# Optimization experiments

Measured on AMD Instinct MI355X. Metric: run time of the kernel, lower is better.

## Reference

```python
import jax, jax.numpy as jnp
import numpy as np

B, L, H, C = 2, 512, 128, 25

def setup_inputs() -> dict:
    key = jax.random.key(0)
    k1, k2, k3, k4 = jax.random.split(key, 4)
    x1 = jax.random.normal(k1, (B, L, H), dtype=jnp.float32)
    x2 = jax.random.normal(k2, (B, L, H), dtype=jnp.float32)
    W = jax.random.normal(k3, (C, 4 * H), dtype=jnp.float32) * (1.0 / np.sqrt(4 * H))
    b = jax.random.normal(k4, (C,), dtype=jnp.float32) * 0.01
    return {"x1": x1, "x2": x2, "W": W, "b": b}

def reference(x1, x2, W, b):
    # feat = cat([x1_i, x2_j, x1_i*x2_j, |x1_i - x2_j|]) over all (i, j) pairs,
    # then Linear(4H -> C). Split W into its 4 H-sized blocks so we never
    # materialize the [B, L, L, 4H] concatenated tensor.
    Hd = x1.shape[-1]
    W1, W2, W3, W4 = (W[:, 0:Hd], W[:, Hd:2*Hd], W[:, 2*Hd:3*Hd], W[:, 3*Hd:4*Hd])
    a = x1[:, :, None, :]   # [B, L, 1, H] -> row token
    c = x2[:, None, :, :]   # [B, 1, L, H] -> col token
    # a@W1 and c@W2 depend on only one index, so compute [B, L, C] then broadcast.
    t1 = jnp.einsum('blh,ch->blc', x1, W1)[:, :, None, :]  # [B, L, 1, C]
    t2 = jnp.einsum('blh,ch->blc', x2, W2)[:, None, :, :]  # [B, 1, L, C]
    # product term is a bilinear contraction; no [B,L,L,H] materialization needed.
    t3 = jnp.einsum('blh,bmh,ch->blmc', x1, x2, W3)         # [B, L, L, C]
    # abs-diff term requires the pairwise [B, L, L, H] tensor (nonlinear in pair).
    t4 = jnp.einsum('blmh,ch->blmc', jnp.abs(a - c), W4)    # [B, L, L, C]
    return t1 + t2 + t3 + t4 + b  # [B, L, L, C]
```

## Files before the change

### kernel.cpp

```cpp
#include <hip/hip_runtime.h>
#include <hip/hip_bf16.h>
#include <math.h>

#define BB 2
#define LL 512
#define HH 128
#define CC 25
#define W4H (4*HH)

typedef __attribute__((ext_vector_type(4))) float    f32x4;
typedef __attribute__((ext_vector_type(8))) _Float16 half8;
typedef __attribute__((ext_vector_type(2))) _Float16 half2t;
typedef __attribute__((ext_vector_type(4))) unsigned uint4v;

#define MTILE 64
#define LPB   8
#define XPH   136

static __device__ __forceinline__ half8 habs8(half8 x) {
    uint4v u = __builtin_bit_cast(uint4v, x);
    u &= 0x7FFF7FFFu;
    return __builtin_bit_cast(half8, u);
}
static __device__ __forceinline__ half2t pkrtz(float a, float b) {
    return __builtin_bit_cast(half2t, __builtin_amdgcn_cvt_pkrtz(a, b));
}
union H4 { half2t h2[2]; unsigned long long u64; };
union H8 { half2t h2[4]; uint4v u4; half8 h8; };

__global__ __launch_bounds__(256)
void biaffine_fused(const float* __restrict__ x1, const float* __restrict__ x2,
                    const float* __restrict__ W, const float* __restrict__ bias,
                    float* __restrict__ out)
{
    __shared__ __align__(16) _Float16 wfrag[2048 * 8];
    __shared__ __align__(16) _Float16 x2h[MTILE * XPH];
    __shared__ __align__(16) _Float16 x1h[LPB * XPH];

    const int tid = threadIdx.x;
    const int b   = blockIdx.z;
    const int l0  = blockIdx.y * LPB;
    const int m0  = blockIdx.x * MTILE;

    const int lane = tid & 63;
    const int wv   = tid >> 6;
    const int q    = lane >> 4;
    const int cn   = lane & 15;

    #pragma unroll
    for (int i = 0; i < 8; ++i) {
        const int fid = i * 256 + tid;
        const int ln  = fid & 63;
        const int t   = (fid >> 6) & 1;
        const int kk  = fid >> 7;
        const int c   = (ln & 15) + 16 * t;
        const int k0  = kk * 32 + ((ln >> 4) << 3);
        const int wc  = (k0 + 256) & 511;
        H8 h; h.u4 = (uint4v){0u, 0u, 0u, 0u};
        if (c < CC) {
            const f32x4 v0 = *(const f32x4*)(W + (size_t)c * W4H + wc);
            const f32x4 v1 = *(const f32x4*)(W + (size_t)c * W4H + wc + 4);
            h.h2[0] = pkrtz(v0[0], v0[1]);
            h.h2[1] = pkrtz(v0[2], v0[3]);
            h.h2[2] = pkrtz(v1[0], v1[1]);
            h.h2[3] = pkrtz(v1[2], v1[3]);
        }
        *(uint4v*)(&wfrag[fid * 8]) = h.u4;
    }

    {
        const float* sx2 = x2 + ((size_t)b * LL + m0) * HH;
        #pragma unroll
        for (int i = 0; i < 8; ++i) {
            const int idx = i * 256 + tid;
            const int r   = idx >> 5;
            const int c4  = idx & 31;
            const f32x4 v = *(const f32x4*)(sx2 + r * HH + c4 * 4);
            H4 h;
            h.h2[0] = pkrtz(v[0], v[1]);
            h.h2[1] = pkrtz(v[2], v[3]);
            *(unsigned long long*)(&x2h[r * XPH + c4 * 4]) = h.u64;
        }
        const float* sx1 = x1 + ((size_t)b * LL + l0) * HH;
        const int r  = tid >> 5;
        const int c4 = tid & 31;
        const f32x4 v = *(const f32x4*)(sx1 + r * HH + c4 * 4);
        H4 h;
        h.h2[0] = pkrtz(v[0], v[1]);
        h.h2[1] = pkrtz(v[2], v[3]);
        *(unsigned long long*)(&x1h[r * XPH + c4 * 4]) = h.u64;
    }
    __syncthreads();

    half8 Bf0[16], Bf1[16];
    #pragma unroll
    for (int kk = 0; kk < 16; ++kk) {
        Bf0[kk] = *(const half8*)(&wfrag[((kk * 2 + 0) * 64 + lane) * 8]);
        Bf1[kk] = *(const half8*)(&wfrag[((kk * 2 + 1) * 64 + lane) * 8]);
    }

    const int mrowA = wv * 16 + cn;
    half8 X2f[4];
    #pragma unroll
    for (int hh = 0; hh < 4; ++hh)
        X2f[hh] = *(const half8*)(&x2h[mrowA * XPH + hh * 32 + q * 8]);

    const float ba = bias[cn];
    const float bb = (cn + 16 < CC) ? bias[cn + 16] : 0.f;

    #pragma unroll
    for (int l = 0; l < LPB; ++l) {
        f32x4 acc0 = {0.f, 0.f, 0.f, 0.f};
        f32x4 acc1 = {0.f, 0.f, 0.f, 0.f};

        #pragma unroll
        for (int hh = 0; hh < 4; ++hh) {
            const half8 a  = *(const half8*)(&x1h[l * XPH + hh * 32 + q * 8]);
            const half8 bq = X2f[hh];
            const half8 Ap = a * bq;
            const half8 Ad = habs8(a - bq);
            acc0 = __builtin_amdgcn_mfma_f32_16x16x32_f16(Ap, Bf0[hh],      acc0, 0, 0, 0);
            acc1 = __builtin_amdgcn_mfma_f32_16x16x32_f16(Ap, Bf1[hh],      acc1, 0, 0, 0);
            acc0 = __builtin_amdgcn_mfma_f32_16x16x32_f16(Ad, Bf0[4 + hh],  acc0, 0, 0, 0);
            acc1 = __builtin_amdgcn_mfma_f32_16x16x32_f16(Ad, Bf1[4 + hh],  acc1, 0, 0, 0);
            acc0 = __builtin_amdgcn_mfma_f32_16x16x32_f16(a,  Bf0[8 + hh],  acc0, 0, 0, 0);
            acc1 = __builtin_amdgcn_mfma_f32_16x16x32_f16(a,  Bf1[8 + hh],  acc1, 0, 0, 0);
            acc0 = __builtin_amdgcn_mfma_f32_16x16x32_f16(bq, Bf0[12 + hh], acc0, 0, 0, 0);
            acc1 = __builtin_amdgcn_mfma_f32_16x16x32_f16(bq, Bf1[12 + hh], acc1, 0, 0, 0);
        }

        const int lg = l0 + l;
        #pragma unroll
        for (int r = 0; r < 4; ++r) {
            const int mg = m0 + wv * 16 + q * 4 + r;
            float* o = out + (((size_t)b * LL + lg) * LL + mg) * CC;
            o[cn] = acc0[r] + ba;
            if (cn + 16 < CC) o[cn + 16] = acc1[r] + bb;
        }
    }
}

extern "C" void kernel_launch(void* const* d_in, const int* in_sizes, int n_in,
                              void* d_out, int out_size, void* d_ws, size_t ws_size,
                              hipStream_t stream) {
    const float* x1   = (const float*)d_in[0];
    const float* x2   = (const float*)d_in[1];
    const float* W    = (const float*)d_in[2];
    const float* bias = (const float*)d_in[3];
    float* out = (float*)d_out;

    dim3 grid(LL / MTILE, LL / LPB, BB);
    biaffine_fused<<<grid, 256, 0, stream>>>(x1, x2, W, bias, out);
}
```

Before: 92.33 us.

## Prepack W fragments in a separate kernel and split channel halves to cut LDS/registers

Moves the fp16 packing of W into a small pre-kernel that writes MFMA-ready fragments to workspace, so the main kernel no longer spends 32KB of LDS and a per-block conversion on W. The main kernel now loops over the two 16-channel halves sequentially, loading only 16 B-fragments at a time from global memory, which halves register pressure and allows launch_bounds(256,4) for higher occupancy. The trade-off is an extra launch, recomputing the A operands (product and abs-diff) twice, and splitting the output stores into two passes with less contiguity.

```diff
diff --git a/kernel.cpp b/kernel.cpp
--- a/kernel.cpp
+++ b/kernel.cpp
@@ -28,12 +28,34 @@
 union H4 { half2t h2[2]; unsigned long long u64; };
 union H8 { half2t h2[4]; uint4v u4; half8 h8; };
 
+
 __global__ __launch_bounds__(256)
+void wpack_kernel(const float* __restrict__ W, _Float16* __restrict__ wsWf)
+{
+    const int fid = blockIdx.x * 256 + threadIdx.x;
+    const int ln  = fid & 63;
+    const int t   = (fid >> 6) & 1;
+    const int kk  = fid >> 7;
+    const int c   = (ln & 15) + 16 * t;
+    const int k0  = kk * 32 + ((ln >> 4) << 3);
+    const int wc  = (k0 + 256) & 511;
+    H8 h; h.u4 = (uint4v){0u, 0u, 0u, 0u};
+    if (c < CC) {
+        const f32x4 v0 = *(const f32x4*)(W + (size_t)c * W4H + wc);
+        const f32x4 v1 = *(const f32x4*)(W + (size_t)c * W4H + wc + 4);
+        h.h2[0] = pkrtz(v0[0], v0[1]);
+        h.h2[1] = pkrtz(v0[2], v0[3]);
+        h.h2[2] = pkrtz(v1[0], v1[1]);
+        h.h2[3] = pkrtz(v1[2], v1[3]);
+    }
+    *(uint4v*)(wsWf + (size_t)fid * 8) = h.u4;
+}
+
+__global__ __launch_bounds__(256, 4)
 void biaffine_fused(const float* __restrict__ x1, const float* __restrict__ x2,
-                    const float* __restrict__ W, const float* __restrict__ bias,
+                    const _Float16* __restrict__ wsWf, const float* __restrict__ bias,
                     float* __restrict__ out)
 {
-    __shared__ __align__(16) _Float16 wfrag[2048 * 8];
     __shared__ __align__(16) _Float16 x2h[MTILE * XPH];
     __shared__ __align__(16) _Float16 x1h[LPB * XPH];
 
@@ -46,27 +68,6 @@
     const int wv   = tid >> 6;
     const int q    = lane >> 4;
     const int cn   = lane & 15;
-
-    #pragma unroll
-    for (int i = 0; i < 8; ++i) {
-        const int fid = i * 256 + tid;
-        const int ln  = fid & 63;
-        const int t   = (fid >> 6) & 1;
-        const int kk  = fid >> 7;
-        const int c   = (ln & 15) + 16 * t;
-        const int k0  = kk * 32 + ((ln >> 4) << 3);
-        const int wc  = (k0 + 256) & 511;
-        H8 h; h.u4 = (uint4v){0u, 0u, 0u, 0u};
-        if (c < CC) {
-            const f32x4 v0 = *(const f32x4*)(W + (size_t)c * W4H + wc);
-            const f32x4 v1 = *(const f32x4*)(W + (size_t)c * W4H + wc + 4);
-            h.h2[0] = pkrtz(v0[0], v0[1]);
-            h.h2[1] = pkrtz(v0[2], v0[3]);
-            h.h2[2] = pkrtz(v1[0], v1[1]);
-            h.h2[3] = pkrtz(v1[2], v1[3]);
-        }
-        *(uint4v*)(&wfrag[fid * 8]) = h.u4;
-    }
 
     {
         const float* sx2 = x2 + ((size_t)b * LL + m0) * HH;
@@ -92,50 +93,46 @@
     }
     __syncthreads();
 
-    half8 Bf0[16], Bf1[16];
-    #pragma unroll
-    for (int kk = 0; kk < 16; ++kk) {
-        Bf0[kk] = *(const half8*)(&wfrag[((kk * 2 + 0) * 64 + lane) * 8]);
-        Bf1[kk] = *(const half8*)(&wfrag[((kk * 2 + 1) * 64 + lane) * 8]);
-    }
-
     const int mrowA = wv * 16 + cn;
     half8 X2f[4];
     #pragma unroll
     for (int hh = 0; hh < 4; ++hh)
         X2f[hh] = *(const half8*)(&x2h[mrowA * XPH + hh * 32 + q * 8]);
 
-    const float ba = bias[cn];
-    const float bb = (cn + 16 < CC) ? bias[cn + 16] : 0.f;
+    for (int t = 0; t < 2; ++t) {
+        half8 Bf[16];
+        #pragma unroll
+        for (int kk = 0; kk < 16; ++kk)
+            Bf[kk] = *(const half8*)(wsWf + ((size_t)(kk * 2 + t) * 64 + lane) * 8);
 
-    #pragma unroll
-    for (int l = 0; l < LPB; ++l) {
-        f32x4 acc0 = {0.f, 0.f, 0.f, 0.f};
-        f32x4 acc1 = {0.f, 0.f, 0.f, 0.f};
+        const int  cg   = cn + 16 * t;
+        const bool cok  = (cg < CC);
+        const float bt  = cok ? bias[cg] : 0.f;
 
         #pragma unroll
-        for (int hh = 0; hh < 4; ++hh) {
-            const half8 a  = *(const half8*)(&x1h[l * XPH + hh * 32 + q * 8]);
-            const half8 bq = X2f[hh];
-            const half8 Ap = a * bq;
-            const half8 Ad = habs8(a - bq);
-            acc0 = __builtin_amdgcn_mfma_f32_16x16x32_f16(Ap, Bf0[hh],      acc0, 0, 0, 0);
-            acc1 = __builtin_amdgcn_mfma_f32_16x16x32_f16(Ap, Bf1[hh],      acc1, 0, 0, 0);
-            acc0 = __builtin_amdgcn_mfma_f32_16x16x32_f16(Ad, Bf0[4 + hh],  acc0, 0, 0, 0);
-            acc1 = __builtin_amdgcn_mfma_f32_16x16x32_f16(Ad, Bf1[4 + hh],  acc1, 0, 0, 0);
-            acc0 = __builtin_amdgcn_mfma_f32_16x16x32_f16(a,  Bf0[8 + hh],  acc0, 0, 0, 0);
-            acc1 = __builtin_amdgcn_mfma_f32_16x16x32_f16(a,  Bf1[8 + hh],  acc1, 0, 0, 0);
-            acc0 = __builtin_amdgcn_mfma_f32_16x16x32_f16(bq, Bf0[12 + hh], acc0, 0, 0, 0);
-            acc1 = __builtin_amdgcn_mfma_f32_16x16x32_f16(bq, Bf1[12 + hh], acc1, 0, 0, 0);
-        }
+        for (int l = 0; l < LPB; ++l) {
+            f32x4 acc0 = {0.f, 0.f, 0.f, 0.f};
 
-        const int lg = l0 + l;
-        #pragma unroll
-        for (int r = 0; r < 4; ++r) {
-            const int mg = m0 + wv * 16 + q * 4 + r;
-            float* o = out + (((size_t)b * LL + lg) * LL + mg) * CC;
-            o[cn] = acc0[r] + ba;
-            if (cn + 16 < CC) o[cn + 16] = acc1[r] + bb;
+            #pragma unroll
+            for (int hh = 0; hh < 4; ++hh) {
+                const half8 a  = *(const half8*)(&x1h[l * XPH + hh * 32 + q * 8]);
+                const half8 bq = X2f[hh];
+                const half8 Ap = a * bq;
+                const half8 Ad = habs8(a - bq);
+                acc0 = __builtin_amdgcn_mfma_f32_16x16x32_f16(Ap, Bf[hh],      acc0, 0, 0, 0);
+                acc0 = __builtin_amdgcn_mfma_f32_16x16x32_f16(Ad, Bf[4 + hh],  acc0, 0, 0, 0);
+                acc0 = __builtin_amdgcn_mfma_f32_16x16x32_f16(a,  Bf[8 + hh],  acc0, 0, 0, 0);
+                acc0 = __builtin_amdgcn_mfma_f32_16x16x32_f16(bq, Bf[12 + hh], acc0, 0, 0, 0);
+            }
+
+            const int lg = l0 + l;
+            if (cok) {
+                #pragma unroll
+                for (int r = 0; r < 4; ++r) {
+                    const int mg = m0 + wv * 16 + q * 4 + r;
+                    out[(((size_t)b * LL + lg) * LL + mg) * CC + cg] = acc0[r] + bt;
+                }
+            }
         }
     }
 }
@@ -148,7 +145,10 @@
     const float* W    = (const float*)d_in[2];
     const float* bias = (const float*)d_in[3];
     float* out = (float*)d_out;
+    _Float16* wsWf = (_Float16*)d_ws;
+
+    wpack_kernel<<<8, 256, 0, stream>>>(W, wsWf);
 
     dim3 grid(LL / MTILE, LL / LPB, BB);
-    biaffine_fused<<<grid, 256, 0, stream>>>(x1, x2, W, bias, out);
+    biaffine_fused<<<grid, 256, 0, stream>>>(x1, x2, wsWf, bias, out);
 }
```

Result: slower. 312.3 us (+238.2%).

## Hoist rank-one x1·W1 and x2·W2 terms out of the per-pair MFMA loop

Applied to the files above, without the earlier changes.

The x1·W1 term depends only on the row index and the x2·W2 term only on the column index. The kernel now computes each of them once per block with small MFMA passes: t1 is stored in LDS together with the bias, and t2 is kept in registers. The per-(l, m) inner loop then runs only the product and abs-diff contractions, which halves its MFMA count. W fragments and x2 are also loaded straight from global memory into registers instead of being staged through LDS. This adds an extra barrier and redundant global W loads per wave.

```diff
diff --git a/kernel.cpp b/kernel.cpp
--- a/kernel.cpp
+++ b/kernel.cpp
@@ -28,14 +28,28 @@
 union H4 { half2t h2[2]; unsigned long long u64; };
 union H8 { half2t h2[4]; uint4v u4; half8 h8; };
 
+static __device__ __forceinline__ half8 loadWfrag(const float* __restrict__ W,
+                                                  int c, int col0) {
+    H8 h; h.u4 = (uint4v){0u, 0u, 0u, 0u};
+    if (c < CC) {
+        const float* p = W + (size_t)c * W4H + col0;
+        const f32x4 v0 = *(const f32x4*)(p);
+        const f32x4 v1 = *(const f32x4*)(p + 4);
+        h.h2[0] = pkrtz(v0[0], v0[1]);
+        h.h2[1] = pkrtz(v0[2], v0[3]);
+        h.h2[2] = pkrtz(v1[0], v1[1]);
+        h.h2[3] = pkrtz(v1[2], v1[3]);
+    }
+    return h.h8;
+}
+
 __global__ __launch_bounds__(256)
 void biaffine_fused(const float* __restrict__ x1, const float* __restrict__ x2,
                     const float* __restrict__ W, const float* __restrict__ bias,
                     float* __restrict__ out)
 {
-    __shared__ __align__(16) _Float16 wfrag[2048 * 8];
-    __shared__ __align__(16) _Float16 x2h[MTILE * XPH];
     __shared__ __align__(16) _Float16 x1h[LPB * XPH];
+    __shared__ __align__(16) float    t1s[LPB * 32];
 
     const int tid = threadIdx.x;
     const int b   = blockIdx.z;
@@ -47,40 +61,7 @@
     const int q    = lane >> 4;
     const int cn   = lane & 15;
 
-    #pragma unroll
-    for (int i = 0; i < 8; ++i) {
-        const int fid = i * 256 + tid;
-        const int ln  = fid & 63;
-        const int t   = (fid >> 6) & 1;
-        const int kk  = fid >> 7;
-        const int c   = (ln & 15) + 16 * t;
-        const int k0  = kk * 32 + ((ln >> 4) << 3);
-        const int wc  = (k0 + 256) & 511;
-        H8 h; h.u4 = (uint4v){0u, 0u, 0u, 0u};
-        if (c < CC) {
-            const f32x4 v0 = *(const f32x4*)(W + (size_t)c * W4H + wc);
-            const f32x4 v1 = *(const f32x4*)(W + (size_t)c * W4H + wc + 4);
-            h.h2[0] = pkrtz(v0[0], v0[1]);
-            h.h2[1] = pkrtz(v0[2], v0[3]);
-            h.h2[2] = pkrtz(v1[0], v1[1]);
-            h.h2[3] = pkrtz(v1[2], v1[3]);
-        }
-        *(uint4v*)(&wfrag[fid * 8]) = h.u4;
-    }
-
     {
-        const float* sx2 = x2 + ((size_t)b * LL + m0) * HH;
-        #pragma unroll
-        for (int i = 0; i < 8; ++i) {
-            const int idx = i * 256 + tid;
-            const int r   = idx >> 5;
-            const int c4  = idx & 31;
-            const f32x4 v = *(const f32x4*)(sx2 + r * HH + c4 * 4);
-            H4 h;
-            h.h2[0] = pkrtz(v[0], v[1]);
-            h.h2[1] = pkrtz(v[2], v[3]);
-            *(unsigned long long*)(&x2h[r * XPH + c4 * 4]) = h.u64;
-        }
         const float* sx1 = x1 + ((size_t)b * LL + l0) * HH;
         const int r  = tid >> 5;
         const int c4 = tid & 31;
@@ -92,26 +73,72 @@
     }
     __syncthreads();
 
-    half8 Bf0[16], Bf1[16];
-    #pragma unroll
-    for (int kk = 0; kk < 16; ++kk) {
-        Bf0[kk] = *(const half8*)(&wfrag[((kk * 2 + 0) * 64 + lane) * 8]);
-        Bf1[kk] = *(const half8*)(&wfrag[((kk * 2 + 1) * 64 + lane) * 8]);
+    const int mrowA = wv * 16 + cn;
+    half8 X2f[4];
+    {
+        const float* px2 = x2 + ((size_t)b * LL + m0 + mrowA) * HH;
+        #pragma unroll
+        for (int hh = 0; hh < 4; ++hh) {
+            const float* p = px2 + hh * 32 + q * 8;
+            const f32x4 v0 = *(const f32x4*)(p);
+            const f32x4 v1 = *(const f32x4*)(p + 4);
+            H8 h;
+            h.h2[0] = pkrtz(v0[0], v0[1]);
+            h.h2[1] = pkrtz(v0[2], v0[3]);
+            h.h2[2] = pkrtz(v1[0], v1[1]);
+            h.h2[3] = pkrtz(v1[2], v1[3]);
+            X2f[hh] = h.h8;
+        }
     }
 
-    const int mrowA = wv * 16 + cn;
-    half8 X2f[4];
+    f32x4 t2a = {0.f,0.f,0.f,0.f}, t2b = {0.f,0.f,0.f,0.f};
     #pragma unroll
-    for (int hh = 0; hh < 4; ++hh)
-        X2f[hh] = *(const half8*)(&x2h[mrowA * XPH + hh * 32 + q * 8]);
+    for (int kk = 0; kk < 4; ++kk) {
+        const int col0 = HH + kk * 32 + q * 8;
+        const half8 b0 = loadWfrag(W, cn,      col0);
+        const half8 b1 = loadWfrag(W, cn + 16, col0);
+        t2a = __builtin_amdgcn_mfma_f32_16x16x32_f16(X2f[kk], b0, t2a, 0, 0, 0);
+        t2b = __builtin_amdgcn_mfma_f32_16x16x32_f16(X2f[kk], b1, t2b, 0, 0, 0);
+    }
 
-    const float ba = bias[cn];
-    const float bb = (cn + 16 < CC) ? bias[cn + 16] : 0.f;
+    if (wv == 0) {
+        f32x4 t1acc0 = {0.f,0.f,0.f,0.f}, t1acc1 = {0.f,0.f,0.f,0.f};
+        #pragma unroll
+        for (int kk = 0; kk < 4; ++kk) {
+            const half8 a1 = *(const half8*)(&x1h[(cn & 7) * XPH + kk * 32 + q * 8]);
+            const int col0 = kk * 32 + q * 8;
+            const half8 b0 = loadWfrag(W, cn,      col0);
+            const half8 b1 = loadWfrag(W, cn + 16, col0);
+            t1acc0 = __builtin_amdgcn_mfma_f32_16x16x32_f16(a1, b0, t1acc0, 0, 0, 0);
+            t1acc1 = __builtin_amdgcn_mfma_f32_16x16x32_f16(a1, b1, t1acc1, 0, 0, 0);
+        }
+        if (q < 2) {
+            const float ba = bias[cn];
+            const float bb = (cn + 16 < CC) ? bias[cn + 16] : 0.f;
+            #pragma unroll
+            for (int r = 0; r < 4; ++r) {
+                const int l = q * 4 + r;
+                t1s[l * 32 + cn]      = t1acc0[r] + ba;
+                t1s[l * 32 + 16 + cn] = t1acc1[r] + bb;
+            }
+        }
+    }
+
+    half8 Bf0[8], Bf1[8];
+    #pragma unroll
+    for (int kk = 0; kk < 8; ++kk) {
+        const int col0 = 2 * HH + kk * 32 + q * 8;
+        Bf0[kk] = loadWfrag(W, cn,      col0);
+        Bf1[kk] = loadWfrag(W, cn + 16, col0);
+    }
+    __syncthreads();
+
+    const bool cok = (cn + 16 < CC);
 
     #pragma unroll
     for (int l = 0; l < LPB; ++l) {
-        f32x4 acc0 = {0.f, 0.f, 0.f, 0.f};
-        f32x4 acc1 = {0.f, 0.f, 0.f, 0.f};
+        f32x4 acc0 = {0.f,0.f,0.f,0.f};
+        f32x4 acc1 = {0.f,0.f,0.f,0.f};
 
         #pragma unroll
         for (int hh = 0; hh < 4; ++hh) {
@@ -119,23 +146,20 @@
             const half8 bq = X2f[hh];
             const half8 Ap = a * bq;
             const half8 Ad = habs8(a - bq);
-            acc0 = __builtin_amdgcn_mfma_f32_16x16x32_f16(Ap, Bf0[hh],      acc0, 0, 0, 0);
-            acc1 = __builtin_amdgcn_mfma_f32_16x16x32_f16(Ap, Bf1[hh],      acc1, 0, 0, 0);
-            acc0 = __builtin_amdgcn_mfma_f32_16x16x32_f16(Ad, Bf0[4 + hh],  acc0, 0, 0, 0);
-            acc1 = __builtin_amdgcn_mfma_f32_16x16x32_f16(Ad, Bf1[4 + hh],  acc1, 0, 0, 0);
-            acc0 = __builtin_amdgcn_mfma_f32_16x16x32_f16(a,  Bf0[8 + hh],  acc0, 0, 0, 0);
-            acc1 = __builtin_amdgcn_mfma_f32_16x16x32_f16(a,  Bf1[8 + hh],  acc1, 0, 0, 0);
-            acc0 = __builtin_amdgcn_mfma_f32_16x16x32_f16(bq, Bf0[12 + hh], acc0, 0, 0, 0);
-            acc1 = __builtin_amdgcn_mfma_f32_16x16x32_f16(bq, Bf1[12 + hh], acc1, 0, 0, 0);
+            acc0 = __builtin_amdgcn_mfma_f32_16x16x32_f16(Ap, Bf0[hh],     acc0, 0, 0, 0);
+            acc1 = __builtin_amdgcn_mfma_f32_16x16x32_f16(Ap, Bf1[hh],     acc1, 0, 0, 0);
+            acc0 = __builtin_amdgcn_mfma_f32_16x16x32_f16(Ad, Bf0[4 + hh], acc0, 0, 0, 0);
+            acc1 = __builtin_amdgcn_mfma_f32_16x16x32_f16(Ad, Bf1[4 + hh], acc1, 0, 0, 0);
         }
 
         const int lg = l0 + l;
+        const float t1a = t1s[l * 32 + cn];
+        const float t1b = t1s[l * 32 + 16 + cn];
+        float* obase = out + (((size_t)b * LL + lg) * LL + (m0 + wv * 16 + q * 4)) * CC + cn;
         #pragma unroll
         for (int r = 0; r < 4; ++r) {
-            const int mg = m0 + wv * 16 + q * 4 + r;
-            float* o = out + (((size_t)b * LL + lg) * LL + mg) * CC;
-            o[cn] = acc0[r] + ba;
-            if (cn + 16 < CC) o[cn + 16] = acc1[r] + bb;
+            obase[(size_t)r * CC] = acc0[r] + t1a + t2a[r];
+            if (cok) obase[(size_t)r * CC + 16] = acc1[r] + t1b + t2b[r];
         }
     }
 }
```

New measurement: 105.1 us. 13.8% more time.
